# Performance work log

Measured on AMD Instinct MI355X. Metric: run time of the kernel, lower is better.

## Reference

```python
import jax, jax.numpy as jnp
import numpy as np

N, H, W, C = 8, 64, 64, 256
GC = 8            # channels per group (gc)
G = C // GC       # groups = 32
K = 3             # deformable kernel size
KK = K * K
DK = 3            # depthwise kernel size for offset/mask branch


def setup_inputs() -> dict:
    key = jax.random.key(0)
    ks = jax.random.split(key, 6)
    s = 0.02
    return {
        "x": jax.random.normal(ks[0], (N, H, W, C), jnp.float32),
        "dw_w": jax.random.normal(ks[1], (DK, DK, 1, C), jnp.float32) * s,
        "dw_b": jnp.zeros((C,), jnp.float32),
        "om_w": jax.random.normal(ks[2], (C, G * KK * 3), jnp.float32) * s,
        "om_b": jnp.zeros((G * KK * 3,), jnp.float32),
        "vp_w": jax.random.normal(ks[3], (C, C), jnp.float32) * s,
        "vp_b": jnp.zeros((C,), jnp.float32),
        "op_w": jax.random.normal(ks[4], (C, C), jnp.float32) * s,  # output_bias=False
    }


def _dcnv4(x, dw_w, dw_b, om_w, om_b, vp_w, vp_b, op_w):
    n, h, w, c = x.shape
    # --- offset/mask branch: depthwise conv then pointwise linear ---
    xdw = jax.lax.conv_general_dilated(
        x, dw_w, window_strides=(1, 1), padding="SAME",
        dimension_numbers=("NHWC", "HWIO", "NHWC"), feature_group_count=c) + dw_b
    om = (xdw @ om_w + om_b).reshape(n, h, w, G, KK * 3)
    offset = om[..., : 2 * KK].reshape(n, h, w, G, KK, 2)  # (dx, dy) per point
    mask = om[..., 2 * KK :]                                # [n,h,w,G,KK], raw (no softmax in v4)

    # --- value projection ---
    value = (x @ vp_w + vp_b).reshape(n, h, w, G, GC)

    # --- sampling locations: pixel + kernel-grid point + learned offset ---
    kg = (jnp.arange(K) - (K - 1) // 2).astype(jnp.float32)
    ky = jnp.repeat(kg, K)   # [KK]
    kx = jnp.tile(kg, K)     # [KK]
    base_y = jnp.arange(h, dtype=jnp.float32).reshape(1, h, 1, 1, 1)
    base_x = jnp.arange(w, dtype=jnp.float32).reshape(1, 1, w, 1, 1)
    py = base_y + ky + offset[..., 1]  # [n,h,w,G,KK]
    px = base_x + kx + offset[..., 0]

    y0 = jnp.floor(py)
    x0 = jnp.floor(px)
    ty = py - y0
    tx = px - x0

    n_idx = jnp.arange(n).reshape(n, 1, 1, 1, 1)
    g_idx = jnp.arange(G).reshape(1, 1, 1, G, 1)

    def gather(yi, xi):
        valid = (yi >= 0) & (yi <= h - 1) & (xi >= 0) & (xi <= w - 1)
        yc = jnp.clip(yi, 0, h - 1).astype(jnp.int32)
        xc = jnp.clip(xi, 0, w - 1).astype(jnp.int32)
        v = value[n_idx, yc, xc, g_idx]          # [n,h,w,G,KK,GC]
        return v * valid[..., None].astype(value.dtype)

    v00 = gather(y0, x0)
    v01 = gather(y0, x0 + 1)
    v10 = gather(y0 + 1, x0)
    v11 = gather(y0 + 1, x0 + 1)

    sampled = ((1 - ty) * (1 - tx))[..., None] * v00 \
            + ((1 - ty) * tx)[..., None] * v01 \
            + (ty * (1 - tx))[..., None] * v10 \
            + (ty * tx)[..., None] * v11        # [n,h,w,G,KK,GC]

    out = jnp.einsum("nhwgkc,nhwgk->nhwgc", sampled, mask).reshape(n, h, w, c)
    return out @ op_w                            # output proj, no bias


def reference(x, dw_w, dw_b, om_w, om_b, vp_w, vp_b, op_w):
    return _dcnv4(x, dw_w, dw_b, om_w, om_b, vp_w, vp_b, op_w)
```

## Files before the change

kernel.cpp:

```cpp
#include <hip/hip_runtime.h>


typedef __bf16 bf16_t;
typedef bf16_t bf16x8 __attribute__((ext_vector_type(8)));
typedef bf16_t bf16x4 __attribute__((ext_vector_type(4)));
typedef float f32x4 __attribute__((ext_vector_type(4)));

namespace {
constexpr int NN = 8, HH = 64, WW = 64, CC = 256;
constexpr int G = 32, GC = 8;
constexpr int NPIX = NN * HH * WW;
}

__device__ __forceinline__ size_t fragIdx(int row, int c) {
  return ((size_t)(row >> 4) * 4096) + ((c >> 5) * 512) + (((c >> 3) & 3) * 128) +
         ((row & 15) * 8) + (c & 7);
}

__global__ __launch_bounds__(256) void convert_weights_kernel(
    const float* __restrict__ om_w, const float* __restrict__ vp_w,
    const float* __restrict__ op_w, bf16_t* __restrict__ om_wG,
    bf16_t* __restrict__ vp_wF, bf16_t* __restrict__ op_wF) {
  __shared__ float s_t[64][65];
  __shared__ float s_w[256][27];
  const int b = blockIdx.x, t = threadIdx.x;
  if (b < 32) {
    const float* src;
    bf16_t* dst;
    int kt, nt;
    if (b < 16) { src = vp_w; dst = vp_wF; kt = b >> 2; nt = b & 3; }
    else        { src = op_w; dst = op_wF; kt = (b - 16) >> 2; nt = (b - 16) & 3; }
    const int nl = t & 63, kh = t >> 6;
    const int n = nt * 64 + nl;
#pragma unroll
    for (int i = 0; i < 16; ++i) {
      const int kl = kh * 16 + i;
      s_t[kl][nl] = src[(size_t)(kt * 64 + kl) * CC + n];
    }
    __syncthreads();
    const int lane = t & 63, kq = lane >> 4, n15 = lane & 15, n16 = t >> 6;
#pragma unroll
    for (int it = 0; it < 2; ++it) {
      bf16x8 v;
#pragma unroll
      for (int j = 0; j < 8; ++j)
        v[j] = (bf16_t)s_t[it * 32 + kq * 8 + j][n16 * 16 + n15];
      const size_t off = (size_t)(nt * 4 + n16) * 4096 + (size_t)(kt * 2 + it) * 512 +
                         kq * 128 + n15 * 8;
      *(bf16x8*)(dst + off) = v;
    }
  } else {
    const int g = b - 32;
#pragma unroll
    for (int j = 0; j < 27; ++j) s_w[t][j] = om_w[(size_t)t * 864 + g * 27 + j];
    __syncthreads();
#pragma unroll
    for (int i = 0; i < 4; ++i) {
      const int chunk = i * 256 + t;
      const int tile = chunk >> 9, ks = (chunk >> 6) & 7, kq = (chunk >> 4) & 3,
                n15 = chunk & 15;
      const int j = tile * 16 + n15;
      bf16x8 v;
#pragma unroll
      for (int cl = 0; cl < 8; ++cl) {
        const int c = ks * 32 + kq * 8 + cl;
        v[cl] = (j < 27) ? (bf16_t)s_w[c][j] : (bf16_t)0.0f;
      }
      *(bf16x8*)(om_wG + ((size_t)g << 13) + (size_t)chunk * 8) = v;
    }
  }
}

__global__ __launch_bounds__(512, 4) void dwconv_value_kernel(
    const float* __restrict__ x, const float* __restrict__ dw_w,
    const float* __restrict__ dw_b, const bf16_t* __restrict__ vp_wF,
    const float* __restrict__ vp_b, bf16_t* __restrict__ xdwF,
    bf16_t* __restrict__ value_g) {
  __shared__ bf16_t s_xf[64 * 256];

  const int t = threadIdx.x;
  const int row = blockIdx.x;
  const int y = row & 63;
  const int img = row >> 6;

  {
    const int cq = (t & 63) * 4;
    const int seg = t >> 6;
    const bool up = (y > 0), dn = (y < HH - 1);
    const float* xrow = x + (size_t)row * WW * CC + cq;

    const float4 bias = *(const float4*)&dw_b[cq];
    float4 dw[9];
#pragma unroll
    for (int i = 0; i < 9; ++i) dw[i] = *(const float4*)&dw_w[(size_t)i * CC + cq];

    const float4 zero = make_float4(0.f, 0.f, 0.f, 0.f);
    auto loadcol = [&](int xx, float4 c[3]) {
      if (xx < 0 || xx >= WW) { c[0] = c[1] = c[2] = zero; return; }
      c[0] = up ? *(const float4*)(xrow + ((size_t)xx - WW) * CC) : zero;
      c[1] = *(const float4*)(xrow + (size_t)xx * CC);
      c[2] = dn ? *(const float4*)(xrow + ((size_t)xx + WW) * CC) : zero;
    };

    const int x0 = seg * 8;
    float4 cm[3], cc[3], cp[3];
    loadcol(x0 - 1, cm);
    loadcol(x0, cc);

    for (int xx = x0; xx < x0 + 8; ++xx) {
      loadcol(xx + 1, cp);
      float4 a = bias;
#pragma unroll
      for (int r = 0; r < 3; ++r) {
        const float4 w0 = dw[r * 3 + 0], w1 = dw[r * 3 + 1], w2 = dw[r * 3 + 2];
        a.x = fmaf(cm[r].x, w0.x, fmaf(cc[r].x, w1.x, fmaf(cp[r].x, w2.x, a.x)));
        a.y = fmaf(cm[r].y, w0.y, fmaf(cc[r].y, w1.y, fmaf(cp[r].y, w2.y, a.y)));
        a.z = fmaf(cm[r].z, w0.z, fmaf(cc[r].z, w1.z, fmaf(cp[r].z, w2.z, a.z)));
        a.w = fmaf(cm[r].w, w0.w, fmaf(cc[r].w, w1.w, fmaf(cp[r].w, w2.w, a.w)));
      }
      const int pix = row * WW + xx;
      bf16x4 av, cv;
      av[0] = (bf16_t)a.x; av[1] = (bf16_t)a.y; av[2] = (bf16_t)a.z; av[3] = (bf16_t)a.w;
      cv[0] = (bf16_t)cc[1].x; cv[1] = (bf16_t)cc[1].y;
      cv[2] = (bf16_t)cc[1].z; cv[3] = (bf16_t)cc[1].w;
      *(bf16x4*)&xdwF[fragIdx(pix, cq)] = av;
      const int lf = (xx >> 4) * 4096 + ((cq >> 5) * 512) + (((cq >> 3) & 3) * 128) +
                     ((xx & 15) * 8) + (cq & 7);
      *(bf16x4*)&s_xf[lf] = cv;
#pragma unroll
      for (int r = 0; r < 3; ++r) { cm[r] = cc[r]; cc[r] = cp[r]; }
    }
  }
  __syncthreads();

  {
    const int lane = t & 63;
    const int wave = t >> 6;
    const int mq = wave >> 1;
    const int nh = wave & 1;
    const int m = lane & 15;
    const int kq = lane >> 4;

    const bf16_t* Ap = s_xf + mq * 4096 + lane * 8;
    const bf16_t* Bp = vp_wF + (size_t)(nh * 8) * 4096 + lane * 8;

    f32x4 acc[8] = {};
#pragma unroll
    for (int ks = 0; ks < 8; ++ks) {
      const bf16x8 a = *(const bf16x8*)(Ap + ks * 512);
#pragma unroll
      for (int i = 0; i < 8; ++i) {
        const bf16x8 b = *(const bf16x8*)(Bp + (size_t)i * 4096 + ks * 512);
        acc[i] = __builtin_amdgcn_mfma_f32_16x16x32_bf16(a, b, acc[i], 0, 0, 0);
      }
    }

#pragma unroll
    for (int i = 0; i < 8; ++i) {
      const int n = (nh * 8 + i) * 16 + m;
      const float bs = vp_b[n];
      const int g = n >> 3, c = n & 7;
      bf16_t* plane = value_g + ((size_t)(img * G + g) << 15) + c;
#pragma unroll
      for (int r = 0; r < 4; ++r) {
        const int pl = mq * 16 + kq * 4 + r;
        const int pin = y * 64 + pl;
        plane[(size_t)pin * GC] = (bf16_t)(acc[i][r] + bs);
      }
    }
  }
}

__global__ __launch_bounds__(512, 2) void oms_kernel(
    const bf16_t* __restrict__ xdwF, const bf16_t* __restrict__ om_wG,
    const float* __restrict__ om_b, const bf16_t* __restrict__ value_g,
    bf16_t* __restrict__ sampledF) {
  __shared__ bf16x8 s_v[66 * 66];
  __shared__ bf16_t s_om[8][4][128][8];

  const int t = threadIdx.x;
  const int lane = t & 63, wave = t >> 6;
  const int b = blockIdx.x;
  const int img = b & 7, g = (b >> 3) & 31, quarter = b >> 8;
  const int c15 = lane & 15, kq = lane >> 4;
  const int tile0 = img * 256 + quarter * 64;

  bf16x8 wf[2][8];
  {
    const bf16_t* base = om_wG + ((size_t)g << 13) + (size_t)lane * 8;
#pragma unroll
    for (int n2 = 0; n2 < 2; ++n2)
#pragma unroll
      for (int ks = 0; ks < 8; ++ks)
        wf[n2][ks] = *(const bf16x8*)(base + n2 * 4096 + ks * 512);
  }
  float bias[2][4];
#pragma unroll
  for (int n2 = 0; n2 < 2; ++n2)
#pragma unroll
    for (int r = 0; r < 4; ++r) {
      const int j = n2 * 16 + kq * 4 + r;
      bias[n2][r] = (j < 27) ? om_b[g * 27 + j] : 0.0f;
    }

  {
    const bf16x8 zv = {};
    for (int i = t; i < 260; i += 512) {
      int Y, X;
      if (i < 66)       { Y = 0;           X = i; }
      else if (i < 132) { Y = 65;          X = i - 66; }
      else if (i < 196) { Y = i - 132 + 1; X = 0; }
      else              { Y = i - 196 + 1; X = 65; }
      s_v[Y * 66 + X] = zv;
    }
    const bf16x8* plane = (const bf16x8*)(value_g + ((size_t)(img * G + g) << 15));
#pragma unroll
    for (int i = 0; i < 8; ++i) {
      const int c = i * 512 + t;
      s_v[((c >> 6) + 1) * 66 + (c & 63) + 1] = plane[c];
    }
  }

  {
    const int tb = tile0 + wave * 8;
#pragma unroll
    for (int q = 0; q < 8; ++q) {
      const bf16_t* Ap = xdwF + ((size_t)(tb + q)) * 4096 + (size_t)lane * 8;
      f32x4 a0 = {}, a1 = {};
#pragma unroll
      for (int ks = 0; ks < 8; ++ks) {
        const bf16x8 xf = *(const bf16x8*)(Ap + ks * 512);
        a0 = __builtin_amdgcn_mfma_f32_16x16x32_bf16(wf[0][ks], xf, a0, 0, 0, 0);
        a1 = __builtin_amdgcn_mfma_f32_16x16x32_bf16(wf[1][ks], xf, a1, 0, 0, 0);
      }
      const int p = q * 16 + c15;
      bf16x4 b0, b1;
#pragma unroll
      for (int r = 0; r < 4; ++r) {
        b0[r] = (bf16_t)(a0[r] + bias[0][r]);
        b1[r] = (bf16_t)(a1[r] + bias[1][r]);
      }
      *(bf16x4*)&s_om[wave][kq >> 1][p][(kq & 1) * 4] = b0;
      *(bf16x4*)&s_om[wave][2 + (kq >> 1)][p][(kq & 1) * 4] = b1;
    }
  }
  __syncthreads();

  {
    const int pinA = quarter * 1024 + wave * 128 + lane;
    const int pinB = pinA + 64;
    float arrA[27], arrB[27];
#pragma unroll
    for (int c = 0; c < 4; ++c) {
      const bf16x8 oA = *(const bf16x8*)&s_om[wave][c][lane][0];
      const bf16x8 oB = *(const bf16x8*)&s_om[wave][c][64 + lane][0];
#pragma unroll
      for (int j = 0; j < 8; ++j) {
        const int idx = c * 8 + j;
        if (idx < 27) { arrA[idx] = (float)oA[j]; arrB[idx] = (float)oB[j]; }
      }
    }
    const int xw = lane;
    const int yA = (pinA >> 6) & 63;
    const int yB = yA + 1;

    float accA[GC], accB[GC];
#pragma unroll
    for (int c = 0; c < GC; ++c) { accA[c] = 0.0f; accB[c] = 0.0f; }

    auto tap = [&](const float* arr, const int y, float* acc, const int k) {
      const float pxf = (float)(xw + (k % 3) - 1) + arr[2 * k];
      const float pyf = (float)(y + (k / 3) - 1) + arr[2 * k + 1];
      const float mk = arr[18 + k];
      const float x0f = floorf(pxf), y0f = floorf(pyf);
      const float tx = pxf - x0f, ty = pyf - y0f;
      const int ix = (int)x0f, iy = (int)y0f;

      const int iX0 = min(max(ix, -1), 64) + 1;
      const int iX1 = min(max(ix + 1, -1), 64) + 1;
      const int iY0 = min(max(iy, -1), 64) + 1;
      const int iY1 = min(max(iy + 1, -1), 64) + 1;

      const bf16x8 v00 = s_v[iY0 * 66 + iX0];
      const bf16x8 v01 = s_v[iY0 * 66 + iX1];
      const bf16x8 v10 = s_v[iY1 * 66 + iX0];
      const bf16x8 v11 = s_v[iY1 * 66 + iX1];

      const float w00 = mk * (1.0f - ty) * (1.0f - tx);
      const float w01 = mk * (1.0f - ty) * tx;
      const float w10 = mk * ty * (1.0f - tx);
      const float w11 = mk * ty * tx;

#pragma unroll
      for (int c = 0; c < GC; ++c) {
        float s = acc[c];
        s = fmaf(w00, (float)v00[c], s);
        s = fmaf(w01, (float)v01[c], s);
        s = fmaf(w10, (float)v10[c], s);
        s = fmaf(w11, (float)v11[c], s);
        acc[c] = s;
      }
    };

#pragma unroll
    for (int k = 0; k < 9; ++k) {
      tap(arrA, yA, accA, k);
      tap(arrB, yB, accB, k);
    }

    bf16x8 svA, svB;
#pragma unroll
    for (int c = 0; c < GC; ++c) {
      svA[c] = (bf16_t)accA[c];
      svB[c] = (bf16_t)accB[c];
    }
    *(bf16x8*)(sampledF + fragIdx(img * 4096 + pinA, g * 8)) = svA;
    *(bf16x8*)(sampledF + fragIdx(img * 4096 + pinB, g * 8)) = svB;
  }
}

__global__ __launch_bounds__(512, 4) void out_gemm_kernel(
    const bf16_t* __restrict__ AF, const bf16_t* __restrict__ BF,
    float* __restrict__ out) {
  const int lane = threadIdx.x & 63;
  const int wave = threadIdx.x >> 6;
  const int mq = wave >> 1;
  const int nh = wave & 1;
  const int mt = blockIdx.x * 4 + mq;
  const int m = lane & 15;
  const int kq = lane >> 4;

  const bf16_t* Ap = AF + (size_t)mt * 4096 + lane * 8;
  const bf16_t* Bp = BF + (size_t)(nh * 8) * 4096 + lane * 8;

  f32x4 acc[8] = {};
#pragma unroll
  for (int ks = 0; ks < 8; ++ks) {
    const bf16x8 a = *(const bf16x8*)(Ap + ks * 512);
#pragma unroll
    for (int i = 0; i < 8; ++i) {
      const bf16x8 b = *(const bf16x8*)(Bp + (size_t)i * 4096 + ks * 512);
      acc[i] = __builtin_amdgcn_mfma_f32_16x16x32_bf16(a, b, acc[i], 0, 0, 0);
    }
  }

#pragma unroll
  for (int i = 0; i < 8; ++i) {
    const int n = (nh * 8 + i) * 16 + m;
#pragma unroll
    for (int r = 0; r < 4; ++r) {
      const int pix = mt * 16 + kq * 4 + r;
      out[(size_t)pix * CC + n] = acc[i][r];
    }
  }
}

extern "C" void kernel_launch(void* const* d_in, const int* in_sizes, int n_in,
                              void* d_out, int out_size, void* d_ws, size_t ws_size,
                              hipStream_t stream) {
  const float* x = (const float*)d_in[0];
  const float* dw_w = (const float*)d_in[1];
  const float* dw_b = (const float*)d_in[2];
  const float* om_w = (const float*)d_in[3];
  const float* om_b = (const float*)d_in[4];
  const float* vp_w = (const float*)d_in[5];
  const float* vp_b = (const float*)d_in[6];
  const float* op_w = (const float*)d_in[7];
  float* out = (float*)d_out;

  char* ws = (char*)d_ws;
  bf16_t* value_g = (bf16_t*)ws;
  bf16_t* xdwF = (bf16_t*)(ws + 16777216);
  bf16_t* sampledF = (bf16_t*)(ws + 33554432);
  bf16_t* om_wG = (bf16_t*)(ws + 50331648);
  bf16_t* vp_wF = (bf16_t*)(ws + 50855936);
  bf16_t* op_wF = (bf16_t*)(ws + 50987008);

  convert_weights_kernel<<<64, 256, 0, stream>>>(om_w, vp_w, op_w,
                                                 om_wG, vp_wF, op_wF);
  dwconv_value_kernel<<<NN * HH, 512, 0, stream>>>(x, dw_w, dw_b, vp_wF, vp_b,
                                                   xdwF, value_g);
  oms_kernel<<<1024, 512, 0, stream>>>(xdwF, om_wG, om_b, value_g, sampledF);
  out_gemm_kernel<<<NPIX / 64, 512, 0, stream>>>(sampledF, op_wF, out);
}
```

Before: 202.9 us.

## Packed bf16 unpack with f32x2 FMAs in sampler; stage op weights in LDS

```diff
diff --git a/kernel.cpp b/kernel.cpp
--- a/kernel.cpp
+++ b/kernel.cpp
@@ -5,6 +5,8 @@
 typedef bf16_t bf16x8 __attribute__((ext_vector_type(8)));
 typedef bf16_t bf16x4 __attribute__((ext_vector_type(4)));
 typedef float f32x4 __attribute__((ext_vector_type(4)));
+typedef float f32x2 __attribute__((ext_vector_type(2)));
+typedef unsigned int u32x4 __attribute__((ext_vector_type(4)));
 
 namespace {
 constexpr int NN = 8, HH = 64, WW = 64, CC = 256;
@@ -15,6 +17,13 @@
 __device__ __forceinline__ size_t fragIdx(int row, int c) {
   return ((size_t)(row >> 4) * 4096) + ((c >> 5) * 512) + (((c >> 3) & 3) * 128) +
          ((row & 15) * 8) + (c & 7);
+}
+
+__device__ __forceinline__ float bf2f_lo(unsigned u) {
+  return __builtin_bit_cast(float, u << 16);
+}
+__device__ __forceinline__ float bf2f_hi(unsigned u) {
+  return __builtin_bit_cast(float, u & 0xffff0000u);
 }
 
 __global__ __launch_bounds__(256) void convert_weights_kernel(
@@ -249,26 +258,25 @@
   {
     const int pinA = quarter * 1024 + wave * 128 + lane;
     const int pinB = pinA + 64;
-    float arrA[27], arrB[27];
+    float arrA[32], arrB[32];
 #pragma unroll
     for (int c = 0; c < 4; ++c) {
-      const bf16x8 oA = *(const bf16x8*)&s_om[wave][c][lane][0];
-      const bf16x8 oB = *(const bf16x8*)&s_om[wave][c][64 + lane][0];
-#pragma unroll
-      for (int j = 0; j < 8; ++j) {
-        const int idx = c * 8 + j;
-        if (idx < 27) { arrA[idx] = (float)oA[j]; arrB[idx] = (float)oB[j]; }
+      const u32x4 oA = *(const u32x4*)&s_om[wave][c][lane][0];
+      const u32x4 oB = *(const u32x4*)&s_om[wave][c][64 + lane][0];
+#pragma unroll
+      for (int h = 0; h < 4; ++h) {
+        const int idx = c * 8 + h * 2;
+        arrA[idx] = bf2f_lo(oA[h]); arrA[idx + 1] = bf2f_hi(oA[h]);
+        arrB[idx] = bf2f_lo(oB[h]); arrB[idx + 1] = bf2f_hi(oB[h]);
       }
     }
     const int xw = lane;
     const int yA = (pinA >> 6) & 63;
     const int yB = yA + 1;
 
-    float accA[GC], accB[GC];
-#pragma unroll
-    for (int c = 0; c < GC; ++c) { accA[c] = 0.0f; accB[c] = 0.0f; }
-
-    auto tap = [&](const float* arr, const int y, float* acc, const int k) {
+    f32x2 accA[4] = {}, accB[4] = {};
+
+    auto tap = [&](const float* arr, const int y, f32x2* acc2, const int k) {
       const float pxf = (float)(xw + (k % 3) - 1) + arr[2 * k];
       const float pyf = (float)(y + (k / 3) - 1) + arr[2 * k + 1];
       const float mk = arr[18 + k];
@@ -281,24 +289,29 @@
       const int iY0 = min(max(iy, -1), 64) + 1;
       const int iY1 = min(max(iy + 1, -1), 64) + 1;
 
-      const bf16x8 v00 = s_v[iY0 * 66 + iX0];
-      const bf16x8 v01 = s_v[iY0 * 66 + iX1];
-      const bf16x8 v10 = s_v[iY1 * 66 + iX0];
-      const bf16x8 v11 = s_v[iY1 * 66 + iX1];
+      const u32x4 c00 = *(const u32x4*)&s_v[iY0 * 66 + iX0];
+      const u32x4 c01 = *(const u32x4*)&s_v[iY0 * 66 + iX1];
+      const u32x4 c10 = *(const u32x4*)&s_v[iY1 * 66 + iX0];
+      const u32x4 c11 = *(const u32x4*)&s_v[iY1 * 66 + iX1];
 
       const float w00 = mk * (1.0f - ty) * (1.0f - tx);
       const float w01 = mk * (1.0f - ty) * tx;
       const float w10 = mk * ty * (1.0f - tx);
       const float w11 = mk * ty * tx;
-
-#pragma unroll
-      for (int c = 0; c < GC; ++c) {
-        float s = acc[c];
-        s = fmaf(w00, (float)v00[c], s);
-        s = fmaf(w01, (float)v01[c], s);
-        s = fmaf(w10, (float)v10[c], s);
-        s = fmaf(w11, (float)v11[c], s);
-        acc[c] = s;
+      const f32x2 W00 = {w00, w00}, W01 = {w01, w01};
+      const f32x2 W10 = {w10, w10}, W11 = {w11, w11};
+
+#pragma unroll
+      for (int pr = 0; pr < 4; ++pr) {
+        f32x2 v;
+        v[0] = bf2f_lo(c00[pr]); v[1] = bf2f_hi(c00[pr]);
+        acc2[pr] = __builtin_elementwise_fma(W00, v, acc2[pr]);
+        v[0] = bf2f_lo(c01[pr]); v[1] = bf2f_hi(c01[pr]);
+        acc2[pr] = __builtin_elementwise_fma(W01, v, acc2[pr]);
+        v[0] = bf2f_lo(c10[pr]); v[1] = bf2f_hi(c10[pr]);
+        acc2[pr] = __builtin_elementwise_fma(W10, v, acc2[pr]);
+        v[0] = bf2f_lo(c11[pr]); v[1] = bf2f_hi(c11[pr]);
+        acc2[pr] = __builtin_elementwise_fma(W11, v, acc2[pr]);
       }
     };
 
@@ -310,28 +323,41 @@
 
     bf16x8 svA, svB;
 #pragma unroll
-    for (int c = 0; c < GC; ++c) {
-      svA[c] = (bf16_t)accA[c];
-      svB[c] = (bf16_t)accB[c];
+    for (int pr = 0; pr < 4; ++pr) {
+      svA[2 * pr] = (bf16_t)accA[pr][0];
+      svA[2 * pr + 1] = (bf16_t)accA[pr][1];
+      svB[2 * pr] = (bf16_t)accB[pr][0];
+      svB[2 * pr + 1] = (bf16_t)accB[pr][1];
     }
     *(bf16x8*)(sampledF + fragIdx(img * 4096 + pinA, g * 8)) = svA;
     *(bf16x8*)(sampledF + fragIdx(img * 4096 + pinB, g * 8)) = svB;
   }
 }
 
-__global__ __launch_bounds__(512, 4) void out_gemm_kernel(
+__global__ __launch_bounds__(1024, 1) void out_gemm_kernel(
     const bf16_t* __restrict__ AF, const bf16_t* __restrict__ BF,
     float* __restrict__ out) {
-  const int lane = threadIdx.x & 63;
-  const int wave = threadIdx.x >> 6;
+  __shared__ bf16_t s_b[CC * CC];
+
+  const int t = threadIdx.x;
+  {
+    const bf16x8* src = (const bf16x8*)BF;
+    bf16x8* dst = (bf16x8*)s_b;
+#pragma unroll
+    for (int i = 0; i < 8; ++i) dst[i * 1024 + t] = src[i * 1024 + t];
+  }
+  __syncthreads();
+
+  const int lane = t & 63;
+  const int wave = t >> 6;
   const int mq = wave >> 1;
   const int nh = wave & 1;
-  const int mt = blockIdx.x * 4 + mq;
+  const int mt = blockIdx.x * 8 + mq;
   const int m = lane & 15;
   const int kq = lane >> 4;
 
   const bf16_t* Ap = AF + (size_t)mt * 4096 + lane * 8;
-  const bf16_t* Bp = BF + (size_t)(nh * 8) * 4096 + lane * 8;
+  const bf16_t* Bp = s_b + (size_t)(nh * 8) * 4096 + lane * 8;
 
   f32x4 acc[8] = {};
 #pragma unroll
@@ -381,5 +407,5 @@
   dwconv_value_kernel<<<NN * HH, 512, 0, stream>>>(x, dw_w, dw_b, vp_wF, vp_b,
                                                    xdwF, value_g);
   oms_kernel<<<1024, 512, 0, stream>>>(xdwF, om_wG, om_b, value_g, sampledF);
-  out_gemm_kernel<<<NPIX / 64, 512, 0, stream>>>(sampledF, op_wF, out);
-}
+  out_gemm_kernel<<<NPIX / 128, 1024, 0, stream>>>(sampledF, op_wF, out);
+}
```

Result: slower. 211.4 us (+4.2%).
